# Performance work log

Measured on AMD Instinct MI355X. Metric: run time of the kernel, lower is better.

The kernel has to match this reference:

```python
import jax, jax.numpy as jnp
import numpy as np
import math

H = 1024  # hidden_dim
NH = 16   # num_heads
HD = H // NH  # head_dim = 64
B, S, C = 2, 2048, 256  # batch, seq_len, cond_len
EPS = 1e-5


def layernorm(x, g, b):
    m = jnp.mean(x, axis=-1, keepdims=True)
    v = jnp.var(x, axis=-1, keepdims=True)
    return (x - m) * jax.lax.rsqrt(v + EPS) * g + b


def apply_rope(x, freqs):
    # x: [b, s, h, d], freqs broadcastable to [b, s, h, d//2]
    cos, sin = jnp.cos(freqs), jnp.sin(freqs)
    x1, x2 = jnp.split(x, 2, axis=-1)
    return jnp.concatenate([x1 * cos - x2 * sin, x2 * cos + x1 * sin], axis=-1)


def setup_inputs() -> dict:
    key = jax.random.key(0)
    ks = jax.random.split(key, 16)
    sc = 0.02
    x = jax.random.normal(ks[0], (B, S, H), jnp.float32)
    # rope freqs: positions * inv_freq over half head dim
    inv_freq = 1.0 / (10000.0 ** (jnp.arange(HD // 2, dtype=jnp.float32) / (HD // 2)))
    rope_freqs = (jnp.arange(S, dtype=jnp.float32)[:, None] * inv_freq[None, :]).reshape(S, 1, HD // 2)
    # causal additive mask [1,1,S,S]
    causal = jnp.tril(jnp.ones((S, S), dtype=bool))
    attention_mask = jnp.where(causal, 0.0, -1e9).astype(jnp.float32)[None, None]
    conditioning = jax.random.normal(ks[1], (B, C, H), jnp.float32)
    conditioning_mask = jnp.zeros((B, 1, 1, C), jnp.float32)
    params = dict(
        ln1_g=jnp.ones((H,)), ln1_b=jnp.zeros((H,)),
        ln2_g=jnp.ones((H,)), ln2_b=jnp.zeros((H,)),
        lnc_g=jnp.ones((H,)), lnc_b=jnp.zeros((H,)),
        w_qkv=jax.random.normal(ks[2], (H, 3 * H)) * sc,
        w_out=jax.random.normal(ks[3], (H, H)) * sc, b_out=jnp.zeros((H,)),
        w_cq=jax.random.normal(ks[4], (H, H)) * sc,
        w_ckv=jax.random.normal(ks[5], (H, 2 * H)) * sc,
        w_cout=jax.random.normal(ks[6], (H, H)) * sc, b_cout=jnp.zeros((H,)),
        w_ff1=jax.random.normal(ks[7], (H, 4 * H)) * sc, b_ff1=jnp.zeros((4 * H,)),
        w_ff2=jax.random.normal(ks[8], (4 * H, H)) * sc, b_ff2=jnp.zeros((H,)),
    )
    return dict(x=x, rope_freqs=rope_freqs, attention_mask=attention_mask,
                conditioning=conditioning, conditioning_mask=conditioning_mask, **params)


def reference(x, rope_freqs, attention_mask, conditioning, conditioning_mask,
              ln1_g, ln1_b, ln2_g, ln2_b, lnc_g, lnc_b,
              w_qkv, w_out, b_out, w_cq, w_ckv, w_cout, b_cout,
              w_ff1, b_ff1, w_ff2, b_ff2):
    scale = 1.0 / math.sqrt(HD)
    # --- causal self-attention ---
    residual = x
    h = layernorm(x, ln1_g, ln1_b)
    qkv = h @ w_qkv  # [b,s,3H]
    q, k, v = jnp.split(qkv, 3, axis=-1)
    q = q.reshape(B, S, NH, HD)
    k = k.reshape(B, S, NH, HD)
    v = v.reshape(B, S, NH, HD)
    q = apply_rope(q, rope_freqs)
    k = apply_rope(k, rope_freqs)
    scores = jnp.einsum('bqhd,bkhd->bhqk', q, k) * scale + attention_mask
    attn = jax.nn.softmax(scores, axis=-1)
    out = jnp.einsum('bhqk,bkhd->bqhd', attn, v).reshape(B, S, H)
    x = residual + out @ w_out + b_out
    # --- cross-attention ---
    residual = x
    h = layernorm(x, lnc_g, lnc_b)
    q = (h @ w_cq).reshape(B, S, NH, HD)
    kv = conditioning @ w_ckv
    k, v = jnp.split(kv, 2, axis=-1)
    k = k.reshape(B, C, NH, HD)
    v = v.reshape(B, C, NH, HD)
    scores = jnp.einsum('bqhd,bkhd->bhqk', q, k) * scale + conditioning_mask
    attn = jax.nn.softmax(scores, axis=-1)
    out = jnp.einsum('bhqk,bkhd->bqhd', attn, v).reshape(B, S, H)
    x = residual + out @ w_cout + b_cout
    # --- FFN ---
    residual = x
    h = layernorm(x, ln2_g, ln2_b)
    h = jax.nn.gelu(h @ w_ff1 + b_ff1, approximate=False)
    x = residual + h @ w_ff2 + b_ff2
    return x
```

## Files before the change

### kernel.cpp

```cpp
#include <hip/hip_runtime.h>

#define HDIM   1024
#define NHEADS 16
#define HEADD  64
#define BATCH  2
#define SEQ    2048
#define CLEN   256
#define NROWS  (BATCH*SEQ)
#define SCALE  0.125f
#define LOG2E  1.44269504088896f

typedef __bf16 bf16x8 __attribute__((ext_vector_type(8)));
typedef float  f32x4  __attribute__((ext_vector_type(4)));

__device__ __forceinline__ unsigned short f2bf(float f) {
  union { __bf16 b; unsigned short u; } x;
  x.b = (__bf16)f;
  return x.u;
}
__device__ __forceinline__ float bf2f(unsigned short u) {
  union { unsigned int u; float f; } x; x.u = ((unsigned int)u) << 16;
  return x.f;
}

__device__ __forceinline__ void gl2lds16(const unsigned short* g, unsigned short* l) {
  __builtin_amdgcn_global_load_lds(
      (const __attribute__((address_space(1))) unsigned int*)g,
      (__attribute__((address_space(3))) unsigned int*)l, 16, 0, 0);
}

template<int VM> __device__ __forceinline__ void wait_vm_barrier() {
  if constexpr (VM == 0)      asm volatile("s_waitcnt vmcnt(0)\n\ts_barrier" ::: "memory");
  else if constexpr (VM == 2) asm volatile("s_waitcnt vmcnt(2)\n\ts_barrier" ::: "memory");
  else if constexpr (VM == 3) asm volatile("s_waitcnt vmcnt(3)\n\ts_barrier" ::: "memory");
  else                        asm volatile("s_waitcnt vmcnt(4)\n\ts_barrier" ::: "memory");
}
__device__ __forceinline__ void bar_only() { asm volatile("s_barrier" ::: "memory"); }

__global__ __launch_bounds__(256)
void cast_transpose64(const float* __restrict__ in, unsigned short* __restrict__ out,
                      int K, int N) {
  __shared__ float t[64][68];
  const int kb = blockIdx.y * 64, nb = blockIdx.x * 64;
  const int tid = threadIdx.x;
  const int r = tid >> 4, c = (tid & 15) * 4;
#pragma unroll
  for (int i = 0; i < 4; ++i) {
    float4 v = *(const float4*)(in + (size_t)(kb + r + i * 16) * N + nb + c);
    t[r + i * 16][c]     = v.x;
    t[r + i * 16][c + 1] = v.y;
    t[r + i * 16][c + 2] = v.z;
    t[r + i * 16][c + 3] = v.w;
  }
  __syncthreads();
  const int nr = tid >> 3, kc = (tid & 7) * 8;
#pragma unroll
  for (int i = 0; i < 2; ++i) {
    unsigned short us[8];
#pragma unroll
    for (int j = 0; j < 8; ++j) us[j] = f2bf(t[kc + j][nr + i * 32]);
    *(uint4*)(out + (size_t)(nb + nr + i * 32) * K + kb + kc) = *(uint4*)us;
  }
}

__global__ void cast_kernel8(const float* __restrict__ in, unsigned short* __restrict__ out, int n8) {
  int i = blockIdx.x * 256 + threadIdx.x;
  if (i < n8) {
    float4 a = ((const float4*)in)[2 * i], b = ((const float4*)in)[2 * i + 1];
    unsigned short us[8] = { f2bf(a.x), f2bf(a.y), f2bf(a.z), f2bf(a.w),
                             f2bf(b.x), f2bf(b.y), f2bf(b.z), f2bf(b.w) };
    ((uint4*)out)[i] = *(uint4*)us;
  }
}

__global__ __launch_bounds__(256)
void vtrans_kernel(const unsigned short* __restrict__ in, int str, int voff, int rows,
                   unsigned short* __restrict__ out) {
  __shared__ unsigned short t[64][72];
  const int h = blockIdx.y & (NHEADS - 1), b = blockIdx.y >> 4;
  const int s0 = blockIdx.x * 64;
  const int tid = threadIdx.x;
  const int r = tid >> 2, c = (tid & 3) * 16;
  const unsigned short* src = in + (size_t)(b * rows + s0 + r) * str + voff + h * 64 + c;
  *(uint4*)(&t[r][c])     = *(const uint4*)(src);
  *(uint4*)(&t[r][c + 8]) = *(const uint4*)(src + 8);
  __syncthreads();
  const int d = tid >> 2, sc = (tid & 3) * 16;
  unsigned short tmp[16];
#pragma unroll
  for (int i = 0; i < 16; ++i) tmp[i] = t[sc + i][d];
  unsigned short* dst = out + ((size_t)(b * NHEADS + h) * 64 + d) * rows + s0 + sc;
  *(uint4*)(dst)     = *(uint4*)(tmp);
  *(uint4*)(dst + 8) = *(uint4*)(tmp + 8);
}

__global__ __launch_bounds__(256)
void layernorm_kernel(const float* __restrict__ x, const float* __restrict__ g,
                      const float* __restrict__ b, unsigned short* __restrict__ out) {
  int row = blockIdx.x;
  const float4 v = ((const float4*)(x + (size_t)row * HDIM))[threadIdx.x];
  float s  = v.x + v.y + v.z + v.w;
  float sq = v.x*v.x + v.y*v.y + v.z*v.z + v.w*v.w;
  for (int o = 32; o; o >>= 1) { s += __shfl_xor(s, o); sq += __shfl_xor(sq, o); }
  __shared__ float rs[4], rq[4];
  int wave = threadIdx.x >> 6;
  if ((threadIdx.x & 63) == 0) { rs[wave] = s; rq[wave] = sq; }
  __syncthreads();
  s  = rs[0] + rs[1] + rs[2] + rs[3];
  sq = rq[0] + rq[1] + rq[2] + rq[3];
  float mean = s * (1.f/HDIM);
  float var  = sq * (1.f/HDIM) - mean*mean;
  float rstd = rsqrtf(var + 1e-5f);
  float4 gg = ((const float4*)g)[threadIdx.x];
  float4 bb = ((const float4*)b)[threadIdx.x];
  ushort4 o;
  o.x = f2bf((v.x - mean) * rstd * gg.x + bb.x);
  o.y = f2bf((v.y - mean) * rstd * gg.y + bb.y);
  o.z = f2bf((v.z - mean) * rstd * gg.z + bb.z);
  o.w = f2bf((v.w - mean) * rstd * gg.w + bb.w);
  ((ushort4*)(out + (size_t)row * HDIM))[threadIdx.x] = o;
}

template<int TBM, int TBN, bool BIAS, bool RES, bool GELU_, bool OUTBF>
__global__ __launch_bounds__(512)
void gemm_bt(const unsigned short* __restrict__ A, const unsigned short* __restrict__ Bt,
             const float* __restrict__ bias, const float* __restrict__ res,
             void* __restrict__ out, int M, int N, int K) {
  constexpr int MR = TBM / 32;
  constexpr int NR = TBN / 64;
  constexpr int AIS = TBM / 64;
  constexpr int BIS = TBN / 64;
  constexpr int LOADS = AIS + BIS;
  __shared__ unsigned short Al[2][TBM * 64];
  __shared__ unsigned short Bl[2][TBN * 64];
  const int tid  = threadIdx.x;
  const int wave = tid >> 6, lane = tid & 63;
  const int wr = wave >> 2, wc = wave & 3;
  const int nwg = gridDim.x * gridDim.y;
  int lin = blockIdx.y * gridDim.x + blockIdx.x;
  lin = (lin & 7) * (nwg >> 3) + (lin >> 3);
  const int m0 = (lin / gridDim.x) * TBM, n0 = (lin % gridDim.x) * TBN;
  const int lrow = lane & 15, hi = lane >> 4;
  const int rx = lrow & 7;

  f32x4 acc[MR][NR] = {};

  const int trow = tid >> 3, pslot = tid & 7;
  const int lcol = (pslot ^ (trow & 7)) * 8;
  const unsigned short* ga = A  + (size_t)(m0 + trow) * K + lcol;
  const unsigned short* gb = Bt + (size_t)(n0 + trow) * K + lcol;
  const int ldst = trow * 64 + pslot * 8;
  const int nt = K >> 6;

  auto stage = [&](int buf, int t) {
    const int k = t << 6;
#pragma unroll
    for (int i = 0; i < AIS; ++i)
      gl2lds16(ga + (size_t)i * 64 * K + k, Al[buf] + ldst + i * 64 * 64);
#pragma unroll
    for (int i = 0; i < BIS; ++i)
      gl2lds16(gb + (size_t)i * 64 * K + k, Bl[buf] + ldst + i * 64 * 64);
  };
  auto compute = [&](int c) {
#pragma unroll
    for (int kk = 0; kk < 2; ++kk) {
      const int cslot = ((kk << 2) | hi);
      const int coff  = (cslot ^ rx) * 8;
      bf16x8 af[MR], bfr[NR];
#pragma unroll
      for (int m = 0; m < MR; ++m)
        af[m] = *(const bf16x8*)(Al[c] + (wr*(TBM/2) + m*16 + lrow) * 64 + coff);
#pragma unroll
      for (int n = 0; n < NR; ++n)
        bfr[n] = *(const bf16x8*)(Bl[c] + (wc*(TBN/4) + n*16 + lrow) * 64 + coff);
#pragma unroll
      for (int m = 0; m < MR; ++m)
#pragma unroll
        for (int n = 0; n < NR; ++n)
          acc[m][n] = __builtin_amdgcn_mfma_f32_16x16x32_bf16(af[m], bfr[n], acc[m][n], 0, 0, 0);
    }
  };

  stage(0, 0);
  int cur = 0;
  for (int t = 0; t < nt - 1; ++t) {
    stage(cur ^ 1, t + 1);
    wait_vm_barrier<LOADS>();
    compute(cur);
    bar_only();
    cur ^= 1;
  }
  wait_vm_barrier<0>();
  compute(cur);

#pragma unroll
  for (int m = 0; m < MR; ++m)
#pragma unroll
    for (int n = 0; n < NR; ++n)
#pragma unroll
      for (int r = 0; r < 4; ++r) {
        int row = m0 + wr*(TBM/2) + m*16 + hi * 4 + r;
        int col = n0 + wc*(TBN/4) + n*16 + lrow;
        float v = acc[m][n][r];
        if (BIAS)  v += bias[col];
        if (GELU_) v = 0.5f * v * (1.0f + erff(v * 0.70710678118654752f));
        if (RES)   v += res[(size_t)row * N + col];
        if (OUTBF) ((unsigned short*)out)[(size_t)row * N + col] = f2bf(v);
        else       ((float*)out)[(size_t)row * N + col] = v;
      }
}

__global__ void rope_kernel(unsigned short* __restrict__ qkv, const float* __restrict__ freqs) {
  int idx = blockIdx.x * 256 + threadIdx.x;
  int d = idx & 31;
  int h = (idx >> 5) & 15;
  int row = idx >> 9;
  int s = row & (SEQ - 1);
  float f = freqs[s * 32 + d];
  float sn, cs;
  sincosf(f, &sn, &cs);
  size_t base = (size_t)row * 3072 + h * 64 + d;
  float x1 = bf2f(qkv[base]), x2 = bf2f(qkv[base + 32]);
  qkv[base]      = f2bf(x1 * cs - x2 * sn);
  qkv[base + 32] = f2bf(x2 * cs + x1 * sn);
  float y1 = bf2f(qkv[base + 1024]), y2 = bf2f(qkv[base + 1024 + 32]);
  qkv[base + 1024]      = f2bf(y1 * cs - y2 * sn);
  qkv[base + 1024 + 32] = f2bf(y2 * cs + y1 * sn);
}

__global__ __launch_bounds__(512)
void flash_attn_causal8(const unsigned short* __restrict__ qp, int qstr,
                        const unsigned short* __restrict__ kp, int kstr,
                        const unsigned short* __restrict__ vt,
                        unsigned short* __restrict__ outp) {
  __shared__ unsigned short Kl[2][64 * 64];
  __shared__ unsigned short Vl[2][64 * 64];
  __shared__ unsigned short Pl[8][16][72];

  const int id = blockIdx.y * gridDim.x + blockIdx.x;
  const int bh = (id & 7) * 4 + ((id >> 3) & 3);
  const int qpair = id >> 5;
  const int h = bh & (NHEADS - 1), b = bh >> 4;

  const int tid = threadIdx.x;
  const int wave = tid >> 6, lane = tid & 63;
  const int grp = wave >> 2, w4 = wave & 3;
  const int lo = lane & 15, hi = lane >> 4;
  const int NQB = SEQ / 64;
  const float SC2 = SCALE * LOG2E;
  float* mb = (float*)&Pl[0][0][0];

  bf16x8 onesf;
#pragma unroll
  for (int j = 0; j < 8; ++j) onesf[j] = (__bf16)1.0f;

  const unsigned short* vbase = vt + (size_t)(b * NHEADS + h) * 64 * SEQ;
  const int g256 = tid & 255;
  const int trow = g256 >> 3, pslot = g256 & 7;
  const int lcol = (pslot ^ (trow & 7)) * 8;
  const int ldst = g256 * 8;
  const int x7 = lo & 7;
  const int c0 = (hi ^ x7) * 8, c1 = ((hi + 4) ^ x7) * 8;

  for (int pass = 0; pass < 2; ++pass) {
    const int qblk = pass == 0 ? qpair : NQB - 1 - qpair;
    const int q0 = qblk * 64;
    const int qw = q0 + w4 * 16;

    bf16x8 qf[2];
    {
      const unsigned short* qb = qp + (size_t)(b * SEQ + qw + lo) * qstr + h * 64 + hi * 8;
      qf[0] = *(const bf16x8*)(qb);
      qf[1] = *(const bf16x8*)(qb + 32);
#pragma unroll
      for (int j = 0; j < 8; ++j) {
        qf[0][j] = (__bf16)((float)qf[0][j] * SC2);
        qf[1][j] = (__bf16)((float)qf[1][j] * SC2);
      }
    }

    f32x4 o_acc[4] = {};
    f32x4 l_acc = {};
    float mrow[4];
#pragma unroll
    for (int r = 0; r < 4; ++r) mrow[r] = -1e30f;

    const int T = qblk + 1;
    const int iters = (T + 1) >> 1;
    for (int it = 0; it < iters; ++it) {
      const int t = 2 * it + grp;
      const bool act = t < T;
      const int j0 = t * 64;
      if (act) {
        const unsigned short* ks = kp + (size_t)(b * SEQ + j0 + trow) * kstr + h * 64 + lcol;
        const unsigned short* vs = vbase + (size_t)trow * SEQ + j0 + lcol;
        gl2lds16(ks, Kl[grp] + ldst);
        gl2lds16(ks + (size_t)32 * kstr, Kl[grp] + ldst + 32 * 64);
        gl2lds16(vs, Vl[grp] + ldst);
        gl2lds16(vs + (size_t)32 * SEQ, Vl[grp] + ldst + 32 * 64);
      }
      __syncthreads();
      if (act) {
        const unsigned short* Kc = Kl[grp];
        const unsigned short* Vc = Vl[grp];
        f32x4 s[4] = {};
#pragma unroll
        for (int n = 0; n < 4; ++n) {
          bf16x8 b0 = *(const bf16x8*)(Kc + (n * 16 + lo) * 64 + c0);
          bf16x8 b1 = *(const bf16x8*)(Kc + (n * 16 + lo) * 64 + c1);
          s[n] = __builtin_amdgcn_mfma_f32_16x16x32_bf16(qf[0], b0, s[n], 0, 0, 0);
          s[n] = __builtin_amdgcn_mfma_f32_16x16x32_bf16(qf[1], b1, s[n], 0, 0, 0);
        }
        if (t == T - 1) {
#pragma unroll
          for (int n = 0; n < 4; ++n)
#pragma unroll
            for (int r = 0; r < 4; ++r)
              if (j0 + n * 16 + lo > qw + hi * 4 + r) s[n][r] = -1e30f;
        }
        float pr[4][4];
#pragma unroll
        for (int r = 0; r < 4; ++r) {
          float mx = fmaxf(fmaxf(s[0][r], s[1][r]), fmaxf(s[2][r], s[3][r]));
          mx = fmaxf(mx, __shfl_xor(mx, 1));
          mx = fmaxf(mx, __shfl_xor(mx, 2));
          mx = fmaxf(mx, __shfl_xor(mx, 4));
          mx = fmaxf(mx, __shfl_xor(mx, 8));
          const float mnew = fmaxf(mrow[r], mx);
          const float corr = exp2f(mrow[r] - mnew);
          mrow[r] = mnew;
          l_acc[r] *= corr;
#pragma unroll
          for (int n = 0; n < 4; ++n)
            pr[n][r] = exp2f(s[n][r] - mnew);
#pragma unroll
          for (int n2 = 0; n2 < 4; ++n2) o_acc[n2][r] *= corr;
        }
#pragma unroll
        for (int n = 0; n < 4; ++n)
#pragma unroll
          for (int r = 0; r < 4; ++r)
            Pl[wave][hi * 4 + r][n * 16 + lo] = f2bf(pr[n][r]);

        bf16x8 pa0 = *(const bf16x8*)(&Pl[wave][lo][hi * 8]);
        bf16x8 pa1 = *(const bf16x8*)(&Pl[wave][lo][32 + hi * 8]);
        l_acc = __builtin_amdgcn_mfma_f32_16x16x32_bf16(pa0, onesf, l_acc, 0, 0, 0);
        l_acc = __builtin_amdgcn_mfma_f32_16x16x32_bf16(pa1, onesf, l_acc, 0, 0, 0);
#pragma unroll
        for (int n = 0; n < 4; ++n) {
          bf16x8 vb0 = *(const bf16x8*)(Vc + (n * 16 + lo) * 64 + c0);
          bf16x8 vb1 = *(const bf16x8*)(Vc + (n * 16 + lo) * 64 + c1);
          o_acc[n] = __builtin_amdgcn_mfma_f32_16x16x32_bf16(pa0, vb0, o_acc[n], 0, 0, 0);
          o_acc[n] = __builtin_amdgcn_mfma_f32_16x16x32_bf16(pa1, vb1, o_acc[n], 0, 0, 0);
        }
      }
      __syncthreads();
    }

    unsigned short* ob = outp + (size_t)(b * SEQ + qw) * HDIM + h * 64;
#pragma unroll
    for (int half = 0; half < 2; ++half) {
      __syncthreads();
      if (grp == 1) {
        float* dst = mb + (w4 * 64 + lane) * 13;
#pragma unroll
        for (int rr = 0; rr < 2; ++rr) {
          int r = half * 2 + rr;
          dst[rr * 6]     = mrow[r];
          dst[rr * 6 + 1] = l_acc[r];
#pragma unroll
          for (int n = 0; n < 4; ++n) dst[rr * 6 + 2 + n] = o_acc[n][r];
        }
      }
      __syncthreads();
      if (grp == 0) {
        const float* s1 = mb + (w4 * 64 + lane) * 13;
#pragma unroll
        for (int rr = 0; rr < 2; ++rr) {
          int r = half * 2 + rr;
          float m1 = s1[rr * 6], l1 = s1[rr * 6 + 1];
          float M  = fmaxf(mrow[r], m1);
          float c0f = exp2f(mrow[r] - M), c1f = exp2f(m1 - M);
          float inv = 1.f / (l_acc[r] * c0f + l1 * c1f);
#pragma unroll
          for (int n = 0; n < 4; ++n) {
            float o = o_acc[n][r] * c0f + s1[rr * 6 + 2 + n] * c1f;
            ob[(size_t)(hi * 4 + r) * HDIM + n * 16 + lo] = f2bf(o * inv);
          }
        }
      }
    }
    __syncthreads();
  }
}

__global__ __launch_bounds__(256)
void flash_attn_cross(const unsigned short* __restrict__ qp, int qstr,
                      const unsigned short* __restrict__ kp, int kstr,
                      const unsigned short* __restrict__ vt,
                      int kvrows,
                      unsigned short* __restrict__ outp) {
  __shared__ unsigned short Kl[2][64 * 64];
  __shared__ unsigned short Vl[2][64 * 64];
  __shared__ unsigned short Pl[4][16][72];

  const int id = blockIdx.y * gridDim.x + blockIdx.x;
  const int bh = (id & 7) * 4 + ((id >> 3) & 3);
  const int qblk = id >> 5;
  const int h = bh & (NHEADS - 1), b = bh >> 4;

  const int tid = threadIdx.x;
  const int wave = tid >> 6, lane = tid & 63;
  const int lo = lane & 15, hi = lane >> 4;
  const float SC2 = SCALE * LOG2E;

  bf16x8 onesf;
#pragma unroll
  for (int j = 0; j < 8; ++j) onesf[j] = (__bf16)1.0f;

  const unsigned short* vbase = vt + (size_t)(b * NHEADS + h) * 64 * kvrows;
  const int trow = tid >> 3, pslot = tid & 7;
  const int lcol = (pslot ^ (trow & 7)) * 8;
  const int ldst = tid * 8;
  const int x7 = lo & 7;
  const int c0 = (hi ^ x7) * 8, c1 = ((hi + 4) ^ x7) * 8;

  const int qw = qblk * 64 + wave * 16;

  bf16x8 qf[2];
  {
    const unsigned short* qb = qp + (size_t)(b * SEQ + qw + lo) * qstr + h * 64 + hi * 8;
    qf[0] = *(const bf16x8*)(qb);
    qf[1] = *(const bf16x8*)(qb + 32);
#pragma unroll
    for (int j = 0; j < 8; ++j) {
      qf[0][j] = (__bf16)((float)qf[0][j] * SC2);
      qf[1][j] = (__bf16)((float)qf[1][j] * SC2);
    }
  }

  f32x4 o_acc[4] = {};
  f32x4 l_acc = {};
  float mrow[4];
#pragma unroll
  for (int r = 0; r < 4; ++r) mrow[r] = -1e30f;

  const int T = kvrows / 64;
  {
    const unsigned short* ks = kp + (size_t)(b * kvrows + trow) * kstr + h * 64 + lcol;
    const unsigned short* vs = vbase + (size_t)trow * kvrows + lcol;
    gl2lds16(ks, Kl[0] + ldst);
    gl2lds16(ks + (size_t)32 * kstr, Kl[0] + ldst + 32 * 64);
    gl2lds16(vs, Vl[0] + ldst);
    gl2lds16(vs + (size_t)32 * kvrows, Vl[0] + ldst + 32 * 64);
  }
  __syncthreads();

  int cur = 0;
  for (int t = 0; t < T; ++t) {
    if (t + 1 < T) {
      const int j1 = (t + 1) * 64;
      const unsigned short* ks = kp + (size_t)(b * kvrows + j1 + trow) * kstr + h * 64 + lcol;
      const unsigned short* vs = vbase + (size_t)trow * kvrows + j1 + lcol;
      gl2lds16(ks, Kl[cur ^ 1] + ldst);
      gl2lds16(ks + (size_t)32 * kstr, Kl[cur ^ 1] + ldst + 32 * 64);
      gl2lds16(vs, Vl[cur ^ 1] + ldst);
      gl2lds16(vs + (size_t)32 * kvrows, Vl[cur ^ 1] + ldst + 32 * 64);
    }
    const unsigned short* Kc = Kl[cur];
    const unsigned short* Vc = Vl[cur];

    f32x4 s[4] = {};
#pragma unroll
    for (int n = 0; n < 4; ++n) {
      bf16x8 b0 = *(const bf16x8*)(Kc + (n * 16 + lo) * 64 + c0);
      bf16x8 b1 = *(const bf16x8*)(Kc + (n * 16 + lo) * 64 + c1);
      s[n] = __builtin_amdgcn_mfma_f32_16x16x32_bf16(qf[0], b0, s[n], 0, 0, 0);
      s[n] = __builtin_amdgcn_mfma_f32_16x16x32_bf16(qf[1], b1, s[n], 0, 0, 0);
    }

    float pr[4][4];
#pragma unroll
    for (int r = 0; r < 4; ++r) {
      float mx = fmaxf(fmaxf(s[0][r], s[1][r]), fmaxf(s[2][r], s[3][r]));
      mx = fmaxf(mx, __shfl_xor(mx, 1));
      mx = fmaxf(mx, __shfl_xor(mx, 2));
      mx = fmaxf(mx, __shfl_xor(mx, 4));
      mx = fmaxf(mx, __shfl_xor(mx, 8));
      const float mnew = fmaxf(mrow[r], mx);
      const float corr = exp2f(mrow[r] - mnew);
      mrow[r] = mnew;
      l_acc[r] *= corr;
#pragma unroll
      for (int n = 0; n < 4; ++n)
        pr[n][r] = exp2f(s[n][r] - mnew);
#pragma unroll
      for (int n2 = 0; n2 < 4; ++n2) o_acc[n2][r] *= corr;
    }

#pragma unroll
    for (int n = 0; n < 4; ++n)
#pragma unroll
      for (int r = 0; r < 4; ++r)
        Pl[wave][hi * 4 + r][n * 16 + lo] = f2bf(pr[n][r]);

    bf16x8 pa0 = *(const bf16x8*)(&Pl[wave][lo][hi * 8]);
    bf16x8 pa1 = *(const bf16x8*)(&Pl[wave][lo][32 + hi * 8]);
    l_acc = __builtin_amdgcn_mfma_f32_16x16x32_bf16(pa0, onesf, l_acc, 0, 0, 0);
    l_acc = __builtin_amdgcn_mfma_f32_16x16x32_bf16(pa1, onesf, l_acc, 0, 0, 0);
#pragma unroll
    for (int n = 0; n < 4; ++n) {
      bf16x8 vb0 = *(const bf16x8*)(Vc + (n * 16 + lo) * 64 + c0);
      bf16x8 vb1 = *(const bf16x8*)(Vc + (n * 16 + lo) * 64 + c1);
      o_acc[n] = __builtin_amdgcn_mfma_f32_16x16x32_bf16(pa0, vb0, o_acc[n], 0, 0, 0);
      o_acc[n] = __builtin_amdgcn_mfma_f32_16x16x32_bf16(pa1, vb1, o_acc[n], 0, 0, 0);
    }
    __syncthreads();
    cur ^= 1;
  }

  unsigned short* ob = outp + (size_t)(b * SEQ + qw) * HDIM + h * 64;
#pragma unroll
  for (int r = 0; r < 4; ++r) {
    const float inv = 1.f / l_acc[r];
#pragma unroll
    for (int n = 0; n < 4; ++n)
      ob[(size_t)(hi * 4 + r) * HDIM + n * 16 + lo] = f2bf(o_acc[n][r] * inv);
  }
}

extern "C" void kernel_launch(void* const* d_in, const int* in_sizes, int n_in,
                              void* d_out, int out_size, void* d_ws, size_t ws_size,
                              hipStream_t stream) {
  const float* x      = (const float*)d_in[0];
  const float* rfreq  = (const float*)d_in[1];
  const float* cond   = (const float*)d_in[3];
  const float* ln1_g  = (const float*)d_in[5];
  const float* ln1_b  = (const float*)d_in[6];
  const float* ln2_g  = (const float*)d_in[7];
  const float* ln2_b  = (const float*)d_in[8];
  const float* lnc_g  = (const float*)d_in[9];
  const float* lnc_b  = (const float*)d_in[10];
  const float* w_qkv  = (const float*)d_in[11];
  const float* w_out  = (const float*)d_in[12];
  const float* b_out  = (const float*)d_in[13];
  const float* w_cq   = (const float*)d_in[14];
  const float* w_ckv  = (const float*)d_in[15];
  const float* w_cout = (const float*)d_in[16];
  const float* b_cout = (const float*)d_in[17];
  const float* w_ff1  = (const float*)d_in[18];
  const float* b_ff1  = (const float*)d_in[19];
  const float* w_ff2  = (const float*)d_in[20];
  const float* b_ff2  = (const float*)d_in[21];

  char* ws = (char*)d_ws;
  size_t off = 0;
  auto alloc = [&](size_t bytes) { size_t r = off; off += (bytes + 255) & ~(size_t)255; return r; };
  unsigned short* wt_qkv  = (unsigned short*)(ws + alloc((size_t)3072*1024*2));
  unsigned short* wt_out  = (unsigned short*)(ws + alloc((size_t)1024*1024*2));
  unsigned short* wt_cq   = (unsigned short*)(ws + alloc((size_t)1024*1024*2));
  unsigned short* wt_ckv  = (unsigned short*)(ws + alloc((size_t)2048*1024*2));
  unsigned short* wt_cout = (unsigned short*)(ws + alloc((size_t)1024*1024*2));
  unsigned short* wt_ff1  = (unsigned short*)(ws + alloc((size_t)4096*1024*2));
  unsigned short* wt_ff2  = (unsigned short*)(ws + alloc((size_t)1024*4096*2));
  unsigned short* condb   = (unsigned short*)(ws + alloc((size_t)512*1024*2));
  unsigned short* hbuf    = (unsigned short*)(ws + alloc((size_t)NROWS*1024*2));
  unsigned short* big     = (unsigned short*)(ws + alloc((size_t)NROWS*4096*2));
  unsigned short* attnb   = (unsigned short*)(ws + alloc((size_t)NROWS*1024*2));
  float*          x1      = (float*)(ws + alloc((size_t)NROWS*1024*4));
  unsigned short* kvc     = (unsigned short*)(ws + alloc((size_t)512*2048*2));
  unsigned short* vts     = (unsigned short*)(ws + alloc((size_t)BATCH*NHEADS*64*SEQ*2));
  unsigned short* vtc     = (unsigned short*)(ws + alloc((size_t)BATCH*NHEADS*64*CLEN*2));
  float*          outf    = (float*)d_out;

  cast_transpose64<<<dim3(48, 16), 256, 0, stream>>>(w_qkv,  wt_qkv,  1024, 3072);
  cast_transpose64<<<dim3(16, 16), 256, 0, stream>>>(w_out,  wt_out,  1024, 1024);
  cast_transpose64<<<dim3(16, 16), 256, 0, stream>>>(w_cq,   wt_cq,   1024, 1024);
  cast_transpose64<<<dim3(32, 16), 256, 0, stream>>>(w_ckv,  wt_ckv,  1024, 2048);
  cast_transpose64<<<dim3(16, 16), 256, 0, stream>>>(w_cout, wt_cout, 1024, 1024);
  cast_transpose64<<<dim3(64, 16), 256, 0, stream>>>(w_ff1,  wt_ff1,  1024, 4096);
  cast_transpose64<<<dim3(16, 64), 256, 0, stream>>>(w_ff2,  wt_ff2,  4096, 1024);
  cast_kernel8<<<(512*1024/8 + 255)/256, 256, 0, stream>>>(cond, condb, 512*1024/8);

  layernorm_kernel<<<NROWS, 256, 0, stream>>>(x, ln1_g, ln1_b, hbuf);
  gemm_bt<128,128,false,false,false,true><<<dim3(3072/128, NROWS/128), 512, 0, stream>>>(
      hbuf, wt_qkv, nullptr, nullptr, big, NROWS, 3072, 1024);
  rope_kernel<<<(NROWS*NHEADS*32)/256, 256, 0, stream>>>(big, rfreq);
  vtrans_kernel<<<dim3(SEQ/64, BATCH*NHEADS), 256, 0, stream>>>(big, 3072, 2048, SEQ, vts);
  flash_attn_causal8<<<dim3(SEQ/64/2, BATCH*NHEADS), 512, 0, stream>>>(
      big, 3072, big + 1024, 3072, vts, attnb);
  gemm_bt<128,64,true,true,false,false><<<dim3(1024/64, NROWS/128), 512, 0, stream>>>(
      attnb, wt_out, b_out, x, x1, NROWS, 1024, 1024);

  layernorm_kernel<<<NROWS, 256, 0, stream>>>(x1, lnc_g, lnc_b, hbuf);
  gemm_bt<128,64,false,false,false,true><<<dim3(1024/64, NROWS/128), 512, 0, stream>>>(
      hbuf, wt_cq, nullptr, nullptr, big, NROWS, 1024, 1024);
  gemm_bt<64,64,false,false,false,true><<<dim3(2048/64, 512/64), 512, 0, stream>>>(
      condb, wt_ckv, nullptr, nullptr, kvc, 512, 2048, 1024);
  vtrans_kernel<<<dim3(CLEN/64, BATCH*NHEADS), 256, 0, stream>>>(kvc, 2048, 1024, CLEN, vtc);
  flash_attn_cross<<<dim3(SEQ/64, BATCH*NHEADS), 256, 0, stream>>>(
      big, 1024, kvc, 2048, vtc, CLEN, attnb);
  gemm_bt<128,64,true,true,false,false><<<dim3(1024/64, NROWS/128), 512, 0, stream>>>(
      attnb, wt_cout, b_cout, x1, outf, NROWS, 1024, 1024);

  layernorm_kernel<<<NROWS, 256, 0, stream>>>(outf, ln2_g, ln2_b, hbuf);
  gemm_bt<128,128,true,false,true,true><<<dim3(4096/128, NROWS/128), 512, 0, stream>>>(
      hbuf, wt_ff1, b_ff1, nullptr, big, NROWS, 4096, 1024);
  gemm_bt<128,64,true,true,false,false><<<dim3(1024/64, NROWS/128), 512, 0, stream>>>(
      big, wt_ff2, b_ff2, outf, outf, NROWS, 1024, 4096);
}
```

Before: 332.4 us.

## Fuse weight cast kernels into one launch and tighten cross-attn KV pipeline

Replaces seven cast-transpose launches and the conditioning cast with a single kernel that picks its task from a block-index table, cutting launch overhead and letting the small jobs fill the GPU together. In the cross-attention kernel, the end-of-tile __syncthreads plus full wait is replaced by a partial vmcnt wait before compute and a bare barrier after it. This lets the next K/V tile's loads overlap the current tile's compute. The partial-wait count must match the four outstanding loads per tile, or the kernel could read stale LDS.

```diff
diff --git a/kernel.cpp b/kernel.cpp
--- a/kernel.cpp
+++ b/kernel.cpp
@@ -37,12 +37,38 @@
 }
 __device__ __forceinline__ void bar_only() { asm volatile("s_barrier" ::: "memory"); }
 
+struct CastTab { const float* s[8]; unsigned short* d[8]; };
+
 __global__ __launch_bounds__(256)
-void cast_transpose64(const float* __restrict__ in, unsigned short* __restrict__ out,
-                      int K, int N) {
+void cast_fused(CastTab tab) {
   __shared__ float t[64][68];
-  const int kb = blockIdx.y * 64, nb = blockIdx.x * 64;
+  const int bid = blockIdx.x;
   const int tid = threadIdx.x;
+  int w, base, K, N;
+  if      (bid < 768)  { w = 0; base = 0;    K = 1024; N = 3072; }
+  else if (bid < 1024) { w = 1; base = 768;  K = 1024; N = 1024; }
+  else if (bid < 1280) { w = 2; base = 1024; K = 1024; N = 1024; }
+  else if (bid < 1792) { w = 3; base = 1280; K = 1024; N = 2048; }
+  else if (bid < 2048) { w = 4; base = 1792; K = 1024; N = 1024; }
+  else if (bid < 3072) { w = 5; base = 2048; K = 1024; N = 4096; }
+  else if (bid < 4096) { w = 6; base = 3072; K = 4096; N = 1024; }
+  else                 { w = 7; base = 4096; K = 0;    N = 0;    }
+  if (w == 7) {
+    const float* in = tab.s[7];
+    unsigned short* out = tab.d[7];
+    int i = (bid - base) * 256 + tid;
+    float4 a = ((const float4*)in)[2 * i], bq = ((const float4*)in)[2 * i + 1];
+    unsigned short us[8] = { f2bf(a.x),  f2bf(a.y),  f2bf(a.z),  f2bf(a.w),
+                             f2bf(bq.x), f2bf(bq.y), f2bf(bq.z), f2bf(bq.w) };
+    ((uint4*)out)[i] = *(uint4*)us;
+    return;
+  }
+  const float* in = tab.s[w];
+  unsigned short* out = tab.d[w];
+  const int lb = bid - base;
+  const int tilesX = N >> 6;
+  const int bx = lb % tilesX, by = lb / tilesX;
+  const int kb = by * 64, nb = bx * 64;
   const int r = tid >> 4, c = (tid & 15) * 4;
 #pragma unroll
   for (int i = 0; i < 4; ++i) {
@@ -60,16 +86,6 @@
 #pragma unroll
     for (int j = 0; j < 8; ++j) us[j] = f2bf(t[kc + j][nr + i * 32]);
     *(uint4*)(out + (size_t)(nb + nr + i * 32) * K + kb + kc) = *(uint4*)us;
-  }
-}
-
-__global__ void cast_kernel8(const float* __restrict__ in, unsigned short* __restrict__ out, int n8) {
-  int i = blockIdx.x * 256 + threadIdx.x;
-  if (i < n8) {
-    float4 a = ((const float4*)in)[2 * i], b = ((const float4*)in)[2 * i + 1];
-    unsigned short us[8] = { f2bf(a.x), f2bf(a.y), f2bf(a.z), f2bf(a.w),
-                             f2bf(b.x), f2bf(b.y), f2bf(b.z), f2bf(b.w) };
-    ((uint4*)out)[i] = *(uint4*)us;
   }
 }
 
@@ -445,31 +461,18 @@
 #pragma unroll
   for (int r = 0; r < 4; ++r) mrow[r] = -1e30f;
 
-  const int T = kvrows / 64;
-  {
-    const unsigned short* ks = kp + (size_t)(b * kvrows + trow) * kstr + h * 64 + lcol;
-    const unsigned short* vs = vbase + (size_t)trow * kvrows + lcol;
-    gl2lds16(ks, Kl[0] + ldst);
-    gl2lds16(ks + (size_t)32 * kstr, Kl[0] + ldst + 32 * 64);
-    gl2lds16(vs, Vl[0] + ldst);
-    gl2lds16(vs + (size_t)32 * kvrows, Vl[0] + ldst + 32 * 64);
-  }
-  __syncthreads();
-
-  int cur = 0;
-  for (int t = 0; t < T; ++t) {
-    if (t + 1 < T) {
-      const int j1 = (t + 1) * 64;
-      const unsigned short* ks = kp + (size_t)(b * kvrows + j1 + trow) * kstr + h * 64 + lcol;
-      const unsigned short* vs = vbase + (size_t)trow * kvrows + j1 + lcol;
-      gl2lds16(ks, Kl[cur ^ 1] + ldst);
-      gl2lds16(ks + (size_t)32 * kstr, Kl[cur ^ 1] + ldst + 32 * 64);
-      gl2lds16(vs, Vl[cur ^ 1] + ldst);
-      gl2lds16(vs + (size_t)32 * kvrows, Vl[cur ^ 1] + ldst + 32 * 64);
-    }
-    const unsigned short* Kc = Kl[cur];
-    const unsigned short* Vc = Vl[cur];
-
+  auto stageKV = [&](int buf, int t) {
+    const int j = t * 64;
+    const unsigned short* ks = kp + (size_t)(b * kvrows + j + trow) * kstr + h * 64 + lcol;
+    const unsigned short* vs = vbase + (size_t)trow * kvrows + j + lcol;
+    gl2lds16(ks, Kl[buf] + ldst);
+    gl2lds16(ks + (size_t)32 * kstr, Kl[buf] + ldst + 32 * 64);
+    gl2lds16(vs, Vl[buf] + ldst);
+    gl2lds16(vs + (size_t)32 * kvrows, Vl[buf] + ldst + 32 * 64);
+  };
+  auto computeTile = [&](int c) {
+    const unsigned short* Kc = Kl[c];
+    const unsigned short* Vc = Vl[c];
     f32x4 s[4] = {};
 #pragma unroll
     for (int n = 0; n < 4; ++n) {
@@ -478,7 +481,6 @@
       s[n] = __builtin_amdgcn_mfma_f32_16x16x32_bf16(qf[0], b0, s[n], 0, 0, 0);
       s[n] = __builtin_amdgcn_mfma_f32_16x16x32_bf16(qf[1], b1, s[n], 0, 0, 0);
     }
-
     float pr[4][4];
 #pragma unroll
     for (int r = 0; r < 4; ++r) {
@@ -497,13 +499,11 @@
 #pragma unroll
       for (int n2 = 0; n2 < 4; ++n2) o_acc[n2][r] *= corr;
     }
-
 #pragma unroll
     for (int n = 0; n < 4; ++n)
 #pragma unroll
       for (int r = 0; r < 4; ++r)
         Pl[wave][hi * 4 + r][n * 16 + lo] = f2bf(pr[n][r]);
-
     bf16x8 pa0 = *(const bf16x8*)(&Pl[wave][lo][hi * 8]);
     bf16x8 pa1 = *(const bf16x8*)(&Pl[wave][lo][32 + hi * 8]);
     l_acc = __builtin_amdgcn_mfma_f32_16x16x32_bf16(pa0, onesf, l_acc, 0, 0, 0);
@@ -515,9 +515,20 @@
       o_acc[n] = __builtin_amdgcn_mfma_f32_16x16x32_bf16(pa0, vb0, o_acc[n], 0, 0, 0);
       o_acc[n] = __builtin_amdgcn_mfma_f32_16x16x32_bf16(pa1, vb1, o_acc[n], 0, 0, 0);
     }
-    __syncthreads();
+  };
+
+  const int T = kvrows / 64;
+  stageKV(0, 0);
+  int cur = 0;
+  for (int t = 0; t < T - 1; ++t) {
+    stageKV(cur ^ 1, t + 1);
+    wait_vm_barrier<4>();
+    computeTile(cur);
+    bar_only();
     cur ^= 1;
   }
+  wait_vm_barrier<0>();
+  computeTile(cur);
 
   unsigned short* ob = outp + (size_t)(b * SEQ + qw) * HDIM + h * 64;
 #pragma unroll
@@ -573,14 +584,16 @@
   unsigned short* vtc     = (unsigned short*)(ws + alloc((size_t)BATCH*NHEADS*64*CLEN*2));
   float*          outf    = (float*)d_out;
 
-  cast_transpose64<<<dim3(48, 16), 256, 0, stream>>>(w_qkv,  wt_qkv,  1024, 3072);
-  cast_transpose64<<<dim3(16, 16), 256, 0, stream>>>(w_out,  wt_out,  1024, 1024);
-  cast_transpose64<<<dim3(16, 16), 256, 0, stream>>>(w_cq,   wt_cq,   1024, 1024);
-  cast_transpose64<<<dim3(32, 16), 256, 0, stream>>>(w_ckv,  wt_ckv,  1024, 2048);
-  cast_transpose64<<<dim3(16, 16), 256, 0, stream>>>(w_cout, wt_cout, 1024, 1024);
-  cast_transpose64<<<dim3(64, 16), 256, 0, stream>>>(w_ff1,  wt_ff1,  1024, 4096);
-  cast_transpose64<<<dim3(16, 64), 256, 0, stream>>>(w_ff2,  wt_ff2,  4096, 1024);
-  cast_kernel8<<<(512*1024/8 + 255)/256, 256, 0, stream>>>(cond, condb, 512*1024/8);
+  CastTab tab;
+  tab.s[0] = w_qkv;  tab.d[0] = wt_qkv;
+  tab.s[1] = w_out;  tab.d[1] = wt_out;
+  tab.s[2] = w_cq;   tab.d[2] = wt_cq;
+  tab.s[3] = w_ckv;  tab.d[3] = wt_ckv;
+  tab.s[4] = w_cout; tab.d[4] = wt_cout;
+  tab.s[5] = w_ff1;  tab.d[5] = wt_ff1;
+  tab.s[6] = w_ff2;  tab.d[6] = wt_ff2;
+  tab.s[7] = cond;   tab.d[7] = condb;
+  cast_fused<<<4352, 256, 0, stream>>>(tab);
 
   layernorm_kernel<<<NROWS, 256, 0, stream>>>(x, ln1_g, ln1_b, hbuf);
   gemm_bt<128,128,false,false,false,true><<<dim3(3072/128, NROWS/128), 512, 0, stream>>>(
```

Measured after the change: 317.3 us. 4.5% less time.
